# Performance work log

Measured on AMD Instinct MI355X. Metric: run time of the kernel, lower is better.

Reference implementation:

```python
import jax, jax.numpy as jnp
import numpy as np

B, C, N = 2, 71, 1024  # batch, cochlear channels, time steps


def _recurrence_expansion(a_0, f, g):
    """a[n+1] = f[n+1]*a[n] + g[n+1]; returns a[1:], shape of f.

    Faithful to mat_mul_recurrence_expansion: cumsum-of-logs plus a
    triangular exp matmul (f must be positive).
    """
    f_cp = jnp.cumsum(jnp.log(f), axis=-1)                      # [B,C,N]
    n = f.shape[-1]
    r = jnp.arange(n)
    # f_mult[i, j] = exp(f_cp[j] - f_cp[i]) for i <= j, else 0
    f_mult = jnp.where(r[:, None] > r[None, :],
                       jnp.zeros((), f_cp.dtype),
                       jnp.exp(f_cp[..., None, :] - f_cp[..., :, None]))  # [B,C,N,N]
    # g[..., None, :] @ f_mult, squeezed: out[j] = sum_{i<=j} g[i]*exp(f_cp[j]-f_cp[i])
    return jnp.exp(f_cp) * a_0[..., None] + jnp.einsum('bcn,bcnm->bcm', g, f_mult)


def _conv_smooth(x, kernel, steps):
    """Repeated small FIR conv along last axis with SYMMETRIC padding.

    Mirrors conv1d_convolver (tf.nn.conv1d = cross-correlation).
    steps is a static Python int, so the loop unrolls under jit.
    """
    ksz = kernel.shape[0]
    pad = (ksz - 1) // 2
    n = x.shape[-1]
    for _ in range(steps):
        xp = jnp.pad(x, [(0, 0)] * (x.ndim - 1) + [(pad, pad)], mode='symmetric')
        x = sum(kernel[k] * xp[..., k:k + n] for k in range(ksz))
    return x


def setup_inputs() -> dict:
    key = jax.random.key(0)
    k1, k2, k3 = jax.random.split(key, 3)
    a_0 = jax.random.normal(k1, (B, C), jnp.float32)
    # f in (0.6, 0.999): positive decaying recurrence coefficients (log must be finite)
    f = jax.random.uniform(k2, (B, C, N), jnp.float32, minval=0.6, maxval=0.999)
    g = 0.01 * jax.random.normal(k3, (B, C, N), jnp.float32)
    kernel = jnp.array([0.25, 0.5, 0.25], jnp.float32)  # 3-tap AGC smoothing FIR
    return {"a_0": a_0, "f": f, "g": g, "kernel": kernel, "steps": 8}


def reference(a_0, f, g, kernel, steps):
    y = _recurrence_expansion(a_0, f, g)      # [B,C,N] recurrence along time
    yt = jnp.swapaxes(y, -1, -2)              # [B,N,C]: smooth across channels
    yt = _conv_smooth(yt, kernel, steps)
    return jnp.swapaxes(yt, -1, -2)           # [B,C,N]
```

## Files before the change

kernel.cpp:

```cpp
#include <hip/hip_runtime.h>

#define BB 2
#define CC 71
#define NN 1024
#define SGRP 4
#define NGRP 18
#define RMAX 20
#define NLOC 512
#define THREADS 512

__global__ __launch_bounds__(THREADS) void carfac_fused(
    const float* __restrict__ a0,
    const float* __restrict__ f,
    const float* __restrict__ g,
    float* __restrict__ out)
{
    __shared__ float ylds[RMAX][NLOC];

    const int bid  = (int)blockIdx.x;
    const int h    = bid & 1;
    const int grp  = (bid >> 1) % NGRP;
    const int b    = bid / (2 * NGRP);
    const int c0   = grp * SGRP;
    const int seff = (CC - c0 < SGRP) ? (CC - c0) : SGRP;
    const int lo   = (c0 - 8 < 0) ? 0 : (c0 - 8);
    const int hi_  = c0 + seff + 7;
    const int hi   = (hi_ > CC - 1) ? (CC - 1) : hi_;
    const int R    = hi - lo + 1;

    const int wave  = (int)(threadIdx.x >> 6);
    const int lane  = (int)(threadIdx.x & 63);
    const int nbase = h * NLOC;

    for (int r = wave; r < R; r += (THREADS / 64)) {
        const int c = lo + r;
        const float* fr = f + (size_t)(b * CC + c) * NN;
        const float* gr = g + (size_t)(b * CC + c) * NN;
        const int base = lane * 16;

        float fl[16], gl[16];
        const float4* f4 = reinterpret_cast<const float4*>(fr + base);
        const float4* g4 = reinterpret_cast<const float4*>(gr + base);
#pragma unroll
        for (int k = 0; k < 4; ++k) {
            float4 fv = f4[k], gv = g4[k];
            fl[4*k+0]=fv.x; fl[4*k+1]=fv.y; fl[4*k+2]=fv.z; fl[4*k+3]=fv.w;
            gl[4*k+0]=gv.x; gl[4*k+1]=gv.y; gl[4*k+2]=gv.z; gl[4*k+3]=gv.w;
        }

        float F = fl[0], G = gl[0];
#pragma unroll
        for (int i = 1; i < 16; ++i) { G = fmaf(fl[i], G, gl[i]); F *= fl[i]; }

#pragma unroll
        for (int d = 1; d < 64; d <<= 1) {
            float Fp = __shfl_up(F, (unsigned)d, 64);
            float Gp = __shfl_up(G, (unsigned)d, 64);
            if (lane >= d) { G = fmaf(F, Gp, G); F *= Fp; }
        }

        const float a0v = a0[b * CC + c];
        float Aend = fmaf(F, a0v, G);
        float ain  = __shfl_up(Aend, 1u, 64);
        if (lane == 0) ain = a0v;

        float a = ain;
#pragma unroll
        for (int i = 0; i < 16; ++i) { a = fmaf(fl[i], a, gl[i]); fl[i] = a; }

        if (base >= nbase && base < nbase + NLOC) {
            float* dst = &ylds[r][base - nbase];
#pragma unroll
            for (int i = 0; i < 16; ++i) dst[i] = fl[i];
        }
    }
    __syncthreads();

    const int n = (int)threadIdx.x;
    const float W[17] = {
        1.f/65536, 16.f/65536, 120.f/65536, 560.f/65536, 1820.f/65536,
        4368.f/65536, 8008.f/65536, 11440.f/65536, 12870.f/65536,
        11440.f/65536, 8008.f/65536, 4368.f/65536, 1820.f/65536,
        560.f/65536, 120.f/65536, 16.f/65536, 1.f/65536 };

    float win[RMAX];
#pragma unroll
    for (int j = 0; j < RMAX; ++j) {
        int cg = c0 - 8 + j;
        cg = (cg < 0) ? (-1 - cg) : cg;
        cg = (cg > CC - 1) ? (2 * CC - 1 - cg) : cg;
        win[j] = ylds[cg - lo][n];
    }
#pragma unroll
    for (int i = 0; i < SGRP; ++i) {
        float acc = 0.f;
#pragma unroll
        for (int k = 0; k < 17; ++k) acc = fmaf(W[k], win[i + k], acc);
        if (c0 + i < CC)
            out[(size_t)(b * CC + c0 + i) * NN + nbase + n] = acc;
    }
}

extern "C" void kernel_launch(void* const* d_in, const int* in_sizes, int n_in,
                              void* d_out, int out_size, void* d_ws, size_t ws_size,
                              hipStream_t stream)
{
    const float* a0 = (const float*)d_in[0];
    const float* f  = (const float*)d_in[1];
    const float* g  = (const float*)d_in[2];
    float* out = (float*)d_out;

    carfac_fused<<<BB * NGRP * 2, THREADS, 0, stream>>>(a0, f, g, out);
}
```

Before: 10.18 us.

## Process full time axis per block with two interleaved channel scans per wave

New measurement: 11.98 us. +17.7%, slower.

```diff
diff --git a/kernel.cpp b/kernel.cpp
--- a/kernel.cpp
+++ b/kernel.cpp
@@ -3,75 +3,99 @@
 #define BB 2
 #define CC 71
 #define NN 1024
-#define SGRP 4
-#define NGRP 18
-#define RMAX 20
-#define NLOC 512
-#define THREADS 512
+#define SGRP 8
+#define NGRP 9
+#define RMAX 24
+#define THREADS 1024
 
-__global__ __launch_bounds__(THREADS) void carfac_fused(
+__global__ __launch_bounds__(THREADS, 1) void carfac_fused(
     const float* __restrict__ a0,
     const float* __restrict__ f,
     const float* __restrict__ g,
     float* __restrict__ out)
 {
-    __shared__ float ylds[RMAX][NLOC];
+    __shared__ float ylds[RMAX][NN];
 
     const int bid  = (int)blockIdx.x;
-    const int h    = bid & 1;
-    const int grp  = (bid >> 1) % NGRP;
-    const int b    = bid / (2 * NGRP);
+    const int grp  = bid % NGRP;
+    const int b    = bid / NGRP;
     const int c0   = grp * SGRP;
-    const int seff = (CC - c0 < SGRP) ? (CC - c0) : SGRP;
-    const int lo   = (c0 - 8 < 0) ? 0 : (c0 - 8);
-    const int hi_  = c0 + seff + 7;
-    const int hi   = (hi_ > CC - 1) ? (CC - 1) : hi_;
-    const int R    = hi - lo + 1;
 
-    const int wave  = (int)(threadIdx.x >> 6);
-    const int lane  = (int)(threadIdx.x & 63);
-    const int nbase = h * NLOC;
+    const int wave = (int)(threadIdx.x >> 6);
+    const int lane = (int)(threadIdx.x & 63);
+    const int base = lane * 16;
 
-    for (int r = wave; r < R; r += (THREADS / 64)) {
-        const int c = lo + r;
-        const float* fr = f + (size_t)(b * CC + c) * NN;
-        const float* gr = g + (size_t)(b * CC + c) * NN;
-        const int base = lane * 16;
+    int ch0 = c0 - 8 + wave;
+    ch0 = ch0 < 0 ? 0 : (ch0 > CC - 1 ? CC - 1 : ch0);
+    int ch1 = c0 - 8 + wave + 16;
+    ch1 = ch1 < 0 ? 0 : (ch1 > CC - 1 ? CC - 1 : ch1);
+    const bool two = (wave < RMAX - 16);
 
-        float fl[16], gl[16];
-        const float4* f4 = reinterpret_cast<const float4*>(fr + base);
-        const float4* g4 = reinterpret_cast<const float4*>(gr + base);
+    const float* f0 = f + (size_t)(b * CC + ch0) * NN + base;
+    const float* g0 = g + (size_t)(b * CC + ch0) * NN + base;
+    const float* f1 = f + (size_t)(b * CC + ch1) * NN + base;
+    const float* g1 = g + (size_t)(b * CC + ch1) * NN + base;
+
+    float fA[16], gA[16], fB[16], gB[16];
+#pragma unroll
+    for (int k = 0; k < 4; ++k) {
+        float4 fv = reinterpret_cast<const float4*>(f0)[k];
+        float4 gv = reinterpret_cast<const float4*>(g0)[k];
+        fA[4*k]=fv.x; fA[4*k+1]=fv.y; fA[4*k+2]=fv.z; fA[4*k+3]=fv.w;
+        gA[4*k]=gv.x; gA[4*k+1]=gv.y; gA[4*k+2]=gv.z; gA[4*k+3]=gv.w;
+    }
+#pragma unroll
+    for (int k = 0; k < 4; ++k) {
+        float4 fv = reinterpret_cast<const float4*>(f1)[k];
+        float4 gv = reinterpret_cast<const float4*>(g1)[k];
+        fB[4*k]=fv.x; fB[4*k+1]=fv.y; fB[4*k+2]=fv.z; fB[4*k+3]=fv.w;
+        gB[4*k]=gv.x; gB[4*k+1]=gv.y; gB[4*k+2]=gv.z; gB[4*k+3]=gv.w;
+    }
+    const float a0v0 = a0[b * CC + ch0];
+    const float a0v1 = a0[b * CC + ch1];
+
+    float F0 = fA[0], G0 = gA[0], F1 = fB[0], G1 = gB[0];
+#pragma unroll
+    for (int i = 1; i < 16; ++i) {
+        G0 = fmaf(fA[i], G0, gA[i]); F0 *= fA[i];
+        G1 = fmaf(fB[i], G1, gB[i]); F1 *= fB[i];
+    }
+#pragma unroll
+    for (int d = 1; d < 64; d <<= 1) {
+        float Fp0 = __shfl_up(F0, (unsigned)d, 64);
+        float Gp0 = __shfl_up(G0, (unsigned)d, 64);
+        float Fp1 = __shfl_up(F1, (unsigned)d, 64);
+        float Gp1 = __shfl_up(G1, (unsigned)d, 64);
+        if (lane >= d) {
+            G0 = fmaf(F0, Gp0, G0); F0 *= Fp0;
+            G1 = fmaf(F1, Gp1, G1); F1 *= Fp1;
+        }
+    }
+    float Ae0 = fmaf(F0, a0v0, G0);
+    float Ae1 = fmaf(F1, a0v1, G1);
+    float ai0 = __shfl_up(Ae0, 1u, 64);
+    float ai1 = __shfl_up(Ae1, 1u, 64);
+    if (lane == 0) { ai0 = a0v0; ai1 = a0v1; }
+
+    float aa = ai0, ab = ai1;
+#pragma unroll
+    for (int i = 0; i < 16; ++i) {
+        aa = fmaf(fA[i], aa, gA[i]); fA[i] = aa;
+        ab = fmaf(fB[i], ab, gB[i]); fB[i] = ab;
+    }
+
+    float4* d0 = reinterpret_cast<float4*>(&ylds[wave][base]);
+#pragma unroll
+    for (int k = 0; k < 4; ++k) {
+        float4 ov; ov.x=fA[4*k]; ov.y=fA[4*k+1]; ov.z=fA[4*k+2]; ov.w=fA[4*k+3];
+        d0[k] = ov;
+    }
+    if (two) {
+        float4* d1 = reinterpret_cast<float4*>(&ylds[wave + 16][base]);
 #pragma unroll
         for (int k = 0; k < 4; ++k) {
-            float4 fv = f4[k], gv = g4[k];
-            fl[4*k+0]=fv.x; fl[4*k+1]=fv.y; fl[4*k+2]=fv.z; fl[4*k+3]=fv.w;
-            gl[4*k+0]=gv.x; gl[4*k+1]=gv.y; gl[4*k+2]=gv.z; gl[4*k+3]=gv.w;
-        }
-
-        float F = fl[0], G = gl[0];
-#pragma unroll
-        for (int i = 1; i < 16; ++i) { G = fmaf(fl[i], G, gl[i]); F *= fl[i]; }
-
-#pragma unroll
-        for (int d = 1; d < 64; d <<= 1) {
-            float Fp = __shfl_up(F, (unsigned)d, 64);
-            float Gp = __shfl_up(G, (unsigned)d, 64);
-            if (lane >= d) { G = fmaf(F, Gp, G); F *= Fp; }
-        }
-
-        const float a0v = a0[b * CC + c];
-        float Aend = fmaf(F, a0v, G);
-        float ain  = __shfl_up(Aend, 1u, 64);
-        if (lane == 0) ain = a0v;
-
-        float a = ain;
-#pragma unroll
-        for (int i = 0; i < 16; ++i) { a = fmaf(fl[i], a, gl[i]); fl[i] = a; }
-
-        if (base >= nbase && base < nbase + NLOC) {
-            float* dst = &ylds[r][base - nbase];
-#pragma unroll
-            for (int i = 0; i < 16; ++i) dst[i] = fl[i];
+            float4 ov; ov.x=fB[4*k]; ov.y=fB[4*k+1]; ov.z=fB[4*k+2]; ov.w=fB[4*k+3];
+            d1[k] = ov;
         }
     }
     __syncthreads();
@@ -89,15 +113,16 @@
         int cg = c0 - 8 + j;
         cg = (cg < 0) ? (-1 - cg) : cg;
         cg = (cg > CC - 1) ? (2 * CC - 1 - cg) : cg;
-        win[j] = ylds[cg - lo][n];
+        win[j] = ylds[cg - c0 + 8][n];
     }
 #pragma unroll
     for (int i = 0; i < SGRP; ++i) {
-        float acc = 0.f;
+        float acc = W[8] * win[i + 8];
 #pragma unroll
-        for (int k = 0; k < 17; ++k) acc = fmaf(W[k], win[i + k], acc);
+        for (int k = 0; k < 8; ++k)
+            acc = fmaf(W[k], win[i + k] + win[i + 16 - k], acc);
         if (c0 + i < CC)
-            out[(size_t)(b * CC + c0 + i) * NN + nbase + n] = acc;
+            out[(size_t)(b * CC + c0 + i) * NN + n] = acc;
     }
 }
 
@@ -110,5 +135,5 @@
     const float* g  = (const float*)d_in[2];
     float* out = (float*)d_out;
 
-    carfac_fused<<<BB * NGRP * 2, THREADS, 0, stream>>>(a0, f, g, out);
+    carfac_fused<<<BB * NGRP, THREADS, 0, stream>>>(a0, f, g, out);
 }
```
